# Kernel tuning notes

Hardware: AMD Instinct MI355X
Metric: run time of the kernel (lower is better)

The kernel has to match this reference:

```python
import jax, jax.numpy as jnp
import numpy as np

N_CELLS, N_GENES, N_EDGES, D = 10000, 2000, 4000000, 64


def setup_inputs() -> dict:
    key = jax.random.key(0)
    ks = jax.random.split(key, 10)
    return {
        "c_feat": jax.random.normal(ks[0], (N_CELLS, D), dtype=jnp.float32),
        "g_feat": jax.random.normal(ks[1], (N_GENES, D), dtype=jnp.float32),
        "cs_factor": jax.random.uniform(ks[2], (N_CELLS, 1), dtype=jnp.float32),
        "gs_factor": jax.random.uniform(ks[3], (N_GENES, 1), dtype=jnp.float32),
        "src": jax.random.randint(ks[4], (N_EDGES,), 0, N_CELLS),
        "dst": jax.random.randint(ks[5], (N_EDGES,), 0, N_GENES),
        "Wm": jax.random.normal(ks[6], (D, 1), dtype=jnp.float32) / np.sqrt(D),
        "bm": jnp.zeros((1,), dtype=jnp.float32),
        "Wd": jax.random.normal(ks[7], (D, 1), dtype=jnp.float32) / np.sqrt(D),
        "bd": jnp.zeros((1,), dtype=jnp.float32),
        "Wp": jax.random.normal(ks[8], (D, 1), dtype=jnp.float32) / np.sqrt(D),
        "bp": jnp.zeros((1,), dtype=jnp.float32),
    }


def reference(c_feat, g_feat, cs_factor, gs_factor, src, dst, Wm, bm, Wd, bd, Wp, bp):
    # Per-edge gather + elementwise product: u_mul_v('h','h','h_d')  -> [E, D]
    h_d = c_feat[src] * g_feat[dst]
    # Per-edge broadcast of node factors: gs from dst gene, cs from src cell -> [E, 1]
    gs = gs_factor[dst]
    cs = cs_factor[src]
    # Tiny Linear(D,1) heads
    mu_ = jax.nn.sigmoid(h_d @ Wm + bm)          # dec_mean
    disp_ = h_d @ Wd + bd                        # dec_disp
    pi = jax.nn.sigmoid(h_d @ Wp + bp)           # dec_pi
    # ZINB activations with clamping
    disp = jnp.clip(jax.nn.softplus(gs * disp_), 1e-4, 1e4)   # DispAct
    mu = cs * jnp.clip(jnp.exp(gs * mu_) - 1.0, 1e-5, 1e6)    # MeanAct scaled by cs
    return (mu, disp, pi)
```

## Files before the change

kernel.cpp:

```cpp
#include <hip/hip_runtime.h>
#include <hip/hip_bf16.h>
#include <hip/hip_fp16.h>


typedef unsigned int u32;
typedef unsigned short u16;
typedef long long i64;
typedef _Float16 v2h __attribute__((ext_vector_type(2)));

__device__ __forceinline__ float us2f(u16 u) { union { u32 i; float f; } v; v.i = ((u32)u) << 16; return v.f; }
__device__ __forceinline__ float lo2f(u32 u) { union { u32 i; float f; } v; v.i = u << 16; return v.f; }
__device__ __forceinline__ float hi2f(u32 u) { union { u32 i; float f; } v; v.i = u & 0xffff0000u; return v.f; }

union H2 { u32 u; __half2 h; v2h v; };

#if defined(__has_builtin)
#if __has_builtin(__builtin_amdgcn_fdot2)
#define HAS_FDOT2 1
#endif
#endif

__device__ __forceinline__ float qadd(float x) {
    int a = __builtin_amdgcn_mov_dpp(__float_as_int(x), 0xB1, 0xF, 0xF, true);
    float s = x + __int_as_float(a);
    int b = __builtin_amdgcn_mov_dpp(__float_as_int(s), 0x4E, 0xF, 0xF, true);
    return s + __int_as_float(b);
}

#define FLAGS_OFF 200
#define WHALF_B   1024
#define CS32_B    2048
#define GS32_B    42048
#define CHALF_B   50176
#define GHALF_B   1330176
#define WS_NEED   1586176

__global__ __launch_bounds__(256) void zinb_prep_all(
    const void* __restrict__ c, const void* __restrict__ g,
    const void* __restrict__ cs, const void* __restrict__ gsp,
    const void* __restrict__ src, const void* __restrict__ dst,
    const void* __restrict__ Wm, const void* __restrict__ bm,
    const void* __restrict__ Wd, const void* __restrict__ bd,
    const void* __restrict__ Wp, const void* __restrict__ bp,
    char* __restrict__ wsb, int nc, int ng, int ncs, int ngs, int E)
{
    __shared__ int sf[12];
    int t = threadIdx.x;
    if (t < 12) sf[t] = 0;
    __syncthreads();
    {
        int bad;
        const u32* pc = (const u32*)c;
        bad = 0; for (int i = t; i < 1024; i += 256) { int ex = (pc[i] >> 7) & 0xFF; if (ex >= 135) bad = 1; }
        if (bad) atomicOr(&sf[0], 1);
        const u32* pg = (const u32*)g;
        bad = 0; for (int i = t; i < 1024; i += 256) { int ex = (pg[i] >> 7) & 0xFF; if (ex >= 135) bad = 1; }
        if (bad) atomicOr(&sf[1], 1);
        const u32* ps = (const u32*)cs;
        bad = 0; for (int i = t; i < 1024; i += 256) { int ex = (ps[i] >> 7) & 0xFF; if (ex >= 135) bad = 1; }
        if (bad) atomicOr(&sf[2], 1);
        const u32* pq = (const u32*)gsp;
        bad = 0; for (int i = t; i < 1000; i += 256) { int ex = (pq[i] >> 7) & 0xFF; if (ex >= 135) bad = 1; }
        if (bad) atomicOr(&sf[3], 1);
        const u32* p4 = (const u32*)src;
        int on = 0, en = 0;
        for (int i = t; i < 1024; i += 256) { if (p4[2 * i + 1] != 0) on = 1; if (p4[2 * i] != 0) en = 1; }
        if (on) atomicOr(&sf[4], 1);
        if (en) atomicOr(&sf[5], 1);
        const u32* p5 = (const u32*)dst;
        on = 0; en = 0;
        for (int i = t; i < 1024; i += 256) { if (p5[2 * i + 1] != 0) on = 1; if (p5[2 * i] != 0) en = 1; }
        if (on) atomicOr(&sf[6], 1);
        if (en) atomicOr(&sf[7], 1);
        if (t < 3) {
            const u32* pw = (t == 0) ? (const u32*)Wm : (t == 1) ? (const u32*)Wd : (const u32*)Wp;
            bad = 0; for (int i = 0; i < 32; ++i) { int ex = (pw[i] >> 7) & 0xFF; if (ex >= 135) bad = 1; }
            if (bad) atomicOr(&sf[8 + t], 1);
        }
    }
    __syncthreads();
    int fc = sf[0], fg = sf[1], fcs = sf[2], fgs = sf[3];

    int i = blockIdx.x * 256 + t;
    __half* ch  = (__half*)(wsb + CHALF_B);
    __half* gh  = (__half*)(wsb + GHALF_B);
    float* cs32 = (float*)(wsb + CS32_B);
    float* gs32 = (float*)(wsb + GS32_B);
    if (i < nc) ch[i] = __float2half(fc ? ((const float*)c)[i] : us2f(((const u16*)c)[i]));
    if (i < ng) gh[i] = __float2half(fg ? ((const float*)g)[i] : us2f(((const u16*)g)[i]));
    if (i < ncs) cs32[i] = fcs ? ((const float*)cs)[i] : us2f(((const u16*)cs)[i]);
    if (i < ngs) gs32[i] = fgs ? ((const float*)gsp)[i] : us2f(((const u16*)gsp)[i]);

    if (blockIdx.x == 0) {
        float* W32 = (float*)wsb;
        int w0 = sf[8], w1 = sf[9], w2 = sf[10];
        if (t < 64) {
            W32[t]       = w0 ? ((const float*)Wm)[t] : us2f(((const u16*)Wm)[t]);
            W32[64 + t]  = w1 ? ((const float*)Wd)[t] : us2f(((const u16*)Wd)[t]);
            W32[128 + t] = w2 ? ((const float*)Wp)[t] : us2f(((const u16*)Wp)[t]);
        } else if (t == 64) {
            W32[192] = w0 ? ((const float*)bm)[0] : us2f(((const u16*)bm)[0]);
            W32[193] = w1 ? ((const float*)bd)[0] : us2f(((const u16*)bd)[0]);
            W32[194] = w2 ? ((const float*)bp)[0] : us2f(((const u16*)bp)[0]);
        }
        __syncthreads();
        __half* wh = (__half*)(wsb + WHALF_B);
        if (t < 192) wh[t] = __float2half(W32[t]);
        if (t == 192) {
            int* flg = (int*)wsb + FLAGS_OFF;
            flg[0] = fc; flg[1] = fg; flg[2] = fcs; flg[3] = fgs;
            flg[4] = (!sf[4] && sf[5]) ? 1 : 0;
            flg[5] = (!sf[6] && sf[7]) ? 1 : 0;
        }
    }
}

__device__ __forceinline__ void slice_dot(const uint4& c0, const uint4& c1,
                                          const uint4& g0, const uint4& g1,
                                          const u32* wm, const u32* wd, const u32* wp,
                                          float& am, float& ad, float& ap) {
    u32 cw[8] = {c0.x, c0.y, c0.z, c0.w, c1.x, c1.y, c1.z, c1.w};
    u32 gw[8] = {g0.x, g0.y, g0.z, g0.w, g1.x, g1.y, g1.z, g1.w};
    am = 0.f; ad = 0.f; ap = 0.f;
    #pragma unroll
    for (int j = 0; j < 8; ++j) {
        H2 a, b, pr, w;
        a.u = cw[j]; b.u = gw[j];
        pr.h = __hmul2(a.h, b.h);
#ifdef HAS_FDOT2
        w.u = wm[j]; am = __builtin_amdgcn_fdot2(pr.v, w.v, am, false);
        w.u = wd[j]; ad = __builtin_amdgcn_fdot2(pr.v, w.v, ad, false);
        w.u = wp[j]; ap = __builtin_amdgcn_fdot2(pr.v, w.v, ap, false);
#else
        float2 pf = __half22float2(pr.h);
        H2 t0, t1, t2; t0.u = wm[j]; t1.u = wd[j]; t2.u = wp[j];
        float2 wmf = __half22float2(t0.h);
        float2 wdf = __half22float2(t1.h);
        float2 wpf = __half22float2(t2.h);
        am = fmaf(pf.x, wmf.x, fmaf(pf.y, wmf.y, am));
        ad = fmaf(pf.x, wdf.x, fmaf(pf.y, wdf.y, ad));
        ap = fmaf(pf.x, wpf.x, fmaf(pf.y, wpf.y, ap));
#endif
    }
}

__device__ __forceinline__ void zinb_epilogue(float Sm, float Sd, float Sp,
                                              float cs, float gs,
                                              float bmv, float bdv, float bpv,
                                              float* out, int E, int e) {
    float mu_ = __builtin_amdgcn_rcpf(1.f + __expf(-(Sm + bmv)));
    float pi  = __builtin_amdgcn_rcpf(1.f + __expf(-(Sp + bpv)));
    float xd  = gs * (Sd + bdv);
    float sp  = fmaxf(xd, 0.f) + __logf(1.f + __expf(-fabsf(xd)));
    float disp = fminf(fmaxf(sp, 1e-4f), 1e4f);
    float em  = __expf(gs * mu_) - 1.f;
    float mu  = cs * fminf(fmaxf(em, 1e-5f), 1e6f);
    out[e]         = mu;
    out[E + e]     = disp;
    out[2 * E + e] = pi;
}

__global__ __launch_bounds__(256) void zinb_fast3(
    const __half* __restrict__ cT, const __half* __restrict__ gT,
    const float* __restrict__ cs32, const float* __restrict__ gs32,
    const void* __restrict__ src, const void* __restrict__ dst,
    const char* __restrict__ wsb, float* __restrict__ out, int E)
{
    const float* W32 = (const float*)wsb;
    const int* flags = (const int*)wsb + FLAGS_OFF;
    int fs64 = flags[4], fd64 = flags[5];

    int tid = threadIdx.x;
    int q = tid >> 2, l = tid & 3;
    int base = blockIdx.x * 256;

    int sI[4], dI[4];
    #pragma unroll
    for (int it = 0; it < 4; ++it) {
        int e = base + it * 64 + q;
        sI[it] = fs64 ? (int)((const i64*)src)[e] : ((const int*)src)[e];
        dI[it] = fd64 ? (int)((const i64*)dst)[e] : ((const int*)dst)[e];
    }
    int s_own = sI[0], d_own = dI[0];
    #pragma unroll
    for (int it = 1; it < 4; ++it) {
        if (l == it) { s_own = sI[it]; d_own = dI[it]; }
    }
    float cs = cs32[s_own];
    float gs = gs32[d_own];

    const uint4* Wh = (const uint4*)(wsb + WHALF_B);
    uint4 m0 = Wh[l],      m1 = Wh[4 + l];
    uint4 d0 = Wh[8 + l],  d1 = Wh[12 + l];
    uint4 p0 = Wh[16 + l], p1 = Wh[20 + l];
    u32 wm[8] = {m0.x, m0.y, m0.z, m0.w, m1.x, m1.y, m1.z, m1.w};
    u32 wd[8] = {d0.x, d0.y, d0.z, d0.w, d1.x, d1.y, d1.z, d1.w};
    u32 wp[8] = {p0.x, p0.y, p0.z, p0.w, p1.x, p1.y, p1.z, p1.w};
    float bmv = W32[192], bdv = W32[193], bpv = W32[194];

    const uint4* cr = (const uint4*)(cT + (size_t)sI[0] * 64);
    const uint4* gr = (const uint4*)(gT + (size_t)dI[0] * 64);
    uint4 c0 = cr[l], c1 = cr[4 + l];
    uint4 g0 = gr[l], g1 = gr[4 + l];

    float Sm = 0.f, Sd = 0.f, Sp = 0.f;
    #pragma unroll
    for (int it = 0; it < 4; ++it) {
        uint4 nc0, nc1, ng0, ng1;
        if (it < 3) {
            const uint4* crn = (const uint4*)(cT + (size_t)sI[it + 1] * 64);
            const uint4* grn = (const uint4*)(gT + (size_t)dI[it + 1] * 64);
            nc0 = crn[l]; nc1 = crn[4 + l];
            ng0 = grn[l]; ng1 = grn[4 + l];
        }
        float am, ad, ap;
        slice_dot(c0, c1, g0, g1, wm, wd, wp, am, ad, ap);
        am = qadd(am); ad = qadd(ad); ap = qadd(ap);
        if (l == it) { Sm = am; Sd = ad; Sp = ap; }
        if (it < 3) { c0 = nc0; c1 = nc1; g0 = ng0; g1 = ng1; }
    }

    int e_own = base + l * 64 + q;
    zinb_epilogue(Sm, Sd, Sp, cs, gs, bmv, bdv, bpv, out, E, e_own);
}

__global__ __launch_bounds__(256) void zinb_fast2t(
    const __half* __restrict__ cT, const __half* __restrict__ gT,
    const float* __restrict__ cs32, const float* __restrict__ gs32,
    const void* __restrict__ src, const void* __restrict__ dst,
    const char* __restrict__ wsb, float* __restrict__ out, int E, int base0)
{
    const float* W32 = (const float*)wsb;
    const int* flags = (const int*)wsb + FLAGS_OFF;
    int fs64 = flags[4], fd64 = flags[5];

    int tid = threadIdx.x;
    int q = tid >> 2, l = tid & 3;
    int base = base0 + blockIdx.x * 256;

    const uint4* Wh = (const uint4*)(wsb + WHALF_B);
    uint4 m0 = Wh[l],      m1 = Wh[4 + l];
    uint4 d0 = Wh[8 + l],  d1 = Wh[12 + l];
    uint4 p0 = Wh[16 + l], p1 = Wh[20 + l];
    u32 wm[8] = {m0.x, m0.y, m0.z, m0.w, m1.x, m1.y, m1.z, m1.w};
    u32 wd[8] = {d0.x, d0.y, d0.z, d0.w, d1.x, d1.y, d1.z, d1.w};
    u32 wp[8] = {p0.x, p0.y, p0.z, p0.w, p1.x, p1.y, p1.z, p1.w};
    float bmv = W32[192], bdv = W32[193], bpv = W32[194];

    float Sm = 0.f, Sd = 0.f, Sp = 0.f;
    int ss = 0, sd2 = 0, se = -1;

    #pragma unroll
    for (int it = 0; it < 4; ++it) {
        int e = base + it * 64 + q;
        bool ok = (e < E);
        int s = 0, d = 0;
        float am = 0.f, ad = 0.f, ap = 0.f;
        if (ok) {
            s = fs64 ? (int)((const i64*)src)[e] : ((const int*)src)[e];
            d = fd64 ? (int)((const i64*)dst)[e] : ((const int*)dst)[e];
            const uint4* cr = (const uint4*)(cT + (size_t)s * 64);
            const uint4* gr = (const uint4*)(gT + (size_t)d * 64);
            uint4 c0 = cr[l], c1 = cr[4 + l];
            uint4 g0 = gr[l], g1 = gr[4 + l];
            slice_dot(c0, c1, g0, g1, wm, wd, wp, am, ad, ap);
        }
        am = qadd(am); ad = qadd(ad); ap = qadd(ap);
        if (l == it && ok) { Sm = am; Sd = ad; Sp = ap; ss = s; sd2 = d; se = e; }
    }

    if (se >= 0)
        zinb_epilogue(Sm, Sd, Sp, cs32[ss], gs32[sd2], bmv, bdv, bpv, out, E, se);
}

__global__ void zinb_detect(const void* c, int nc, const void* g, int ng,
                            const void* cs, int ncs, const void* gsp, int ngs,
                            const void* src, int ns, const void* dst, int nd,
                            int* flags) {
    __shared__ int s_a, s_b;
    int b = blockIdx.x, t = threadIdx.x;
    if (t == 0) { s_a = 0; s_b = 0; }
    __syncthreads();
    if (b < 4) {
        const u32* p; int n;
        if (b == 0)      { p = (const u32*)c;   n = nc;  }
        else if (b == 1) { p = (const u32*)g;   n = ng;  }
        else if (b == 2) { p = (const u32*)cs;  n = ncs; }
        else             { p = (const u32*)gsp; n = ngs; }
        int words = n / 2; if (words > 16384) words = 16384;
        int bad = 0;
        for (int i = t; i < words; i += 256) { int ex = (p[i] >> 7) & 0xFF; if (ex >= 135) bad = 1; }
        if (bad) atomicOr(&s_a, 1);
        __syncthreads();
        if (t == 0) flags[b] = s_a;
    } else {
        const u32* p = (b == 4) ? (const u32*)src : (const u32*)dst;
        int n = (b == 4) ? ns : nd;
        int pairs = (n < 4096) ? n / 2 : 2048;
        int oddnz = 0, evennz = 0;
        for (int i = t; i < pairs; i += 256) {
            if (p[2 * i + 1] != 0) oddnz = 1;
            if (p[2 * i] != 0)     evennz = 1;
        }
        if (oddnz)  atomicOr(&s_a, 1);
        if (evennz) atomicOr(&s_b, 1);
        __syncthreads();
        if (t == 0) flags[b] = (!s_a && s_b) ? 1 : 0;
    }
}

__global__ void zinb_prep_w(const void* Wm, const void* bm, const void* Wd,
                            const void* bd, const void* Wp, const void* bp,
                            float* W) {
    __shared__ int wf[3];
    int t = threadIdx.x;
    if (t < 3) {
        const u32* p = (t == 0) ? (const u32*)Wm : (t == 1) ? (const u32*)Wd : (const u32*)Wp;
        int bad = 0;
        for (int i = 0; i < 32; ++i) { int ex = (p[i] >> 7) & 0xFF; if (ex >= 135) bad = 1; }
        wf[t] = bad;
    }
    __syncthreads();
    if (t < 64) {
        W[t]       = wf[0] ? ((const float*)Wm)[t] : us2f(((const u16*)Wm)[t]);
        W[64 + t]  = wf[1] ? ((const float*)Wd)[t] : us2f(((const u16*)Wd)[t]);
        W[128 + t] = wf[2] ? ((const float*)Wp)[t] : us2f(((const u16*)Wp)[t]);
    } else if (t == 64) {
        W[192] = wf[0] ? ((const float*)bm)[0] : us2f(((const u16*)bm)[0]);
        W[193] = wf[1] ? ((const float*)bd)[0] : us2f(((const u16*)bd)[0]);
        W[194] = wf[2] ? ((const float*)bp)[0] : us2f(((const u16*)bp)[0]);
    }
}

__global__ __launch_bounds__(256) void zinb_main(
    const void* __restrict__ c_feat, const void* __restrict__ g_feat,
    const void* __restrict__ cs_f, const void* __restrict__ gs_f,
    const void* __restrict__ src, const void* __restrict__ dst,
    const float* __restrict__ W, float* __restrict__ out, int E)
{
    int e = blockIdx.x * 256 + threadIdx.x;
    if (e >= E) return;
    const int* flags = (const int*)W + FLAGS_OFF;
    int fc = flags[0], fg = flags[1], fcs = flags[2], fgs = flags[3];
    int fs64 = flags[4], fd64 = flags[5];
    int s = fs64 ? (int)((const i64*)src)[e] : ((const int*)src)[e];
    int d = fd64 ? (int)((const i64*)dst)[e] : ((const int*)dst)[e];
    const char* crow = (const char*)c_feat + (size_t)s * (fc ? 256 : 128);
    const char* grow = (const char*)g_feat + (size_t)d * (fg ? 256 : 128);
    float accm = 0.f, accd = 0.f, accp = 0.f;
    for (int ch = 0; ch < 4; ++ch) {
        float cb[16], gb[16];
        if (fc) {
            const float4* qq = (const float4*)crow;
            #pragma unroll
            for (int j4 = 0; j4 < 4; ++j4) {
                float4 v = qq[ch * 4 + j4];
                cb[j4 * 4] = v.x; cb[j4 * 4 + 1] = v.y; cb[j4 * 4 + 2] = v.z; cb[j4 * 4 + 3] = v.w;
            }
        } else {
            const uint4* qq = (const uint4*)crow;
            #pragma unroll
            for (int j2 = 0; j2 < 2; ++j2) {
                uint4 v = qq[ch * 2 + j2];
                u32 w[4] = {v.x, v.y, v.z, v.w};
                #pragma unroll
                for (int j = 0; j < 4; ++j) {
                    cb[j2 * 8 + j * 2] = lo2f(w[j]); cb[j2 * 8 + j * 2 + 1] = hi2f(w[j]);
                }
            }
        }
        if (fg) {
            const float4* qq = (const float4*)grow;
            #pragma unroll
            for (int j4 = 0; j4 < 4; ++j4) {
                float4 v = qq[ch * 4 + j4];
                gb[j4 * 4] = v.x; gb[j4 * 4 + 1] = v.y; gb[j4 * 4 + 2] = v.z; gb[j4 * 4 + 3] = v.w;
            }
        } else {
            const uint4* qq = (const uint4*)grow;
            #pragma unroll
            for (int j2 = 0; j2 < 2; ++j2) {
                uint4 v = qq[ch * 2 + j2];
                u32 w[4] = {v.x, v.y, v.z, v.w};
                #pragma unroll
                for (int j = 0; j < 4; ++j) {
                    gb[j2 * 8 + j * 2] = lo2f(w[j]); gb[j2 * 8 + j * 2 + 1] = hi2f(w[j]);
                }
            }
        }
        #pragma unroll
        for (int j = 0; j < 16; ++j) {
            int k = ch * 16 + j;
            float h = cb[j] * gb[j];
            accm = fmaf(h, W[k], accm);
            accd = fmaf(h, W[64 + k], accd);
            accp = fmaf(h, W[128 + k], accp);
        }
    }
    float cs = fcs ? ((const float*)cs_f)[s] : us2f(((const u16*)cs_f)[s]);
    float gs = fgs ? ((const float*)gs_f)[d] : us2f(((const u16*)gs_f)[d]);
    float bmv = W[192], bdv = W[193], bpv = W[194];
    float mu_ = 1.f / (1.f + expf(-(accm + bmv)));
    float pi  = 1.f / (1.f + expf(-(accp + bpv)));
    float xd  = gs * (accd + bdv);
    float sp  = fmaxf(xd, 0.f) + log1pf(expf(-fabsf(xd)));
    float disp = fminf(fmaxf(sp, 1e-4f), 1e4f);
    float em  = expf(gs * mu_) - 1.f;
    float mu  = cs * fminf(fmaxf(em, 1e-5f), 1e6f);
    out[e] = mu; out[E + e] = disp; out[2 * E + e] = pi;
}

extern "C" void kernel_launch(void* const* d_in, const int* in_sizes, int n_in,
                              void* d_out, int out_size, void* d_ws, size_t ws_size,
                              hipStream_t stream) {
    const void* c_feat = d_in[0];
    const void* g_feat = d_in[1];
    const void* cs_f   = d_in[2];
    const void* gs_f   = d_in[3];
    const void* src    = d_in[4];
    const void* dst    = d_in[5];
    const void* Wm     = d_in[6];
    const void* bm     = d_in[7];
    const void* Wd     = d_in[8];
    const void* bd     = d_in[9];
    const void* Wp     = d_in[10];
    const void* bp     = d_in[11];

    int E = in_sizes[4];
    int nc = in_sizes[0], ng = in_sizes[1], ncs = in_sizes[2], ngs = in_sizes[3];
    char* wsb = (char*)d_ws;

    if (ws_size >= (size_t)WS_NEED) {
        int nmax = nc > ng ? nc : ng;
        int prep_blocks = (nmax + 255) / 256;
        zinb_prep_all<<<prep_blocks, 256, 0, stream>>>(
            c_feat, g_feat, cs_f, gs_f, src, dst,
            Wm, bm, Wd, bd, Wp, bp, wsb, nc, ng, ncs, ngs, E);

        const __half* cT = (const __half*)(wsb + CHALF_B);
        const __half* gT = (const __half*)(wsb + GHALF_B);
        const float* cs32 = (const float*)(wsb + CS32_B);
        const float* gs32 = (const float*)(wsb + GS32_B);

        int full_blocks = E / 256;
        if (full_blocks > 0)
            zinb_fast3<<<full_blocks, 256, 0, stream>>>(cT, gT, cs32, gs32, src, dst,
                                                        wsb, (float*)d_out, E);
        int tail = E - full_blocks * 256;
        if (tail > 0)
            zinb_fast2t<<<1, 256, 0, stream>>>(cT, gT, cs32, gs32, src, dst,
                                               wsb, (float*)d_out, E, full_blocks * 256);
    } else {
        float* W = (float*)d_ws;
        int* flags = (int*)W + FLAGS_OFF;
        zinb_detect<<<6, 256, 0, stream>>>(c_feat, nc, g_feat, ng, cs_f, ncs,
                                           gs_f, ngs, src, E, dst, in_sizes[5], flags);
        zinb_prep_w<<<1, 256, 0, stream>>>(Wm, bm, Wd, bd, Wp, bp, W);
        int blocks = (E + 255) / 256;
        zinb_main<<<blocks, 256, 0, stream>>>(c_feat, g_feat, cs_f, gs_f, src, dst,
                                              W, (float*)d_out, E);
    }
}
```

Measured before the change: 195.3 us.

## Split prep into detect/vectorized convert, fp16 scale factors, 4 tiles per block

Replaces the combined prep kernel with a single-block detect kernel and a separate vectorized conversion kernel that converts four elements per thread. Cell and gene scale factors are now stored as fp16 instead of fp32. The main kernel processes four 256-edge tiles per block to amortize weight loading and reduce block count. This adds a kernel launch and reduces precision of the scale factors, which may affect accuracy.

```diff
diff --git a/kernel.cpp b/kernel.cpp
--- a/kernel.cpp
+++ b/kernel.cpp
@@ -29,20 +29,20 @@
 
 #define FLAGS_OFF 200
 #define WHALF_B   1024
-#define CS32_B    2048
-#define GS32_B    42048
-#define CHALF_B   50176
-#define GHALF_B   1330176
-#define WS_NEED   1586176
-
-__global__ __launch_bounds__(256) void zinb_prep_all(
+#define CSH_B     2048
+#define GSH_B     22528
+#define CHALF_B   28672
+#define GHALF_B   1308672
+#define WS_NEED   1564672
+
+__global__ __launch_bounds__(256) void zinb_detect1(
     const void* __restrict__ c, const void* __restrict__ g,
     const void* __restrict__ cs, const void* __restrict__ gsp,
     const void* __restrict__ src, const void* __restrict__ dst,
     const void* __restrict__ Wm, const void* __restrict__ bm,
     const void* __restrict__ Wd, const void* __restrict__ bd,
     const void* __restrict__ Wp, const void* __restrict__ bp,
-    char* __restrict__ wsb, int nc, int ng, int ncs, int ngs, int E)
+    char* __restrict__ wsb, int ngs)
 {
     __shared__ int sf[12];
     int t = threadIdx.x;
@@ -60,7 +60,8 @@
         bad = 0; for (int i = t; i < 1024; i += 256) { int ex = (ps[i] >> 7) & 0xFF; if (ex >= 135) bad = 1; }
         if (bad) atomicOr(&sf[2], 1);
         const u32* pq = (const u32*)gsp;
-        bad = 0; for (int i = t; i < 1000; i += 256) { int ex = (pq[i] >> 7) & 0xFF; if (ex >= 135) bad = 1; }
+        int wq = ngs / 2; if (wq > 1000) wq = 1000;
+        bad = 0; for (int i = t; i < wq; i += 256) { int ex = (pq[i] >> 7) & 0xFF; if (ex >= 135) bad = 1; }
         if (bad) atomicOr(&sf[3], 1);
         const u32* p4 = (const u32*)src;
         int on = 0, en = 0;
@@ -79,40 +80,64 @@
         }
     }
     __syncthreads();
-    int fc = sf[0], fg = sf[1], fcs = sf[2], fgs = sf[3];
-
-    int i = blockIdx.x * 256 + t;
-    __half* ch  = (__half*)(wsb + CHALF_B);
-    __half* gh  = (__half*)(wsb + GHALF_B);
-    float* cs32 = (float*)(wsb + CS32_B);
-    float* gs32 = (float*)(wsb + GS32_B);
-    if (i < nc) ch[i] = __float2half(fc ? ((const float*)c)[i] : us2f(((const u16*)c)[i]));
-    if (i < ng) gh[i] = __float2half(fg ? ((const float*)g)[i] : us2f(((const u16*)g)[i]));
-    if (i < ncs) cs32[i] = fcs ? ((const float*)cs)[i] : us2f(((const u16*)cs)[i]);
-    if (i < ngs) gs32[i] = fgs ? ((const float*)gsp)[i] : us2f(((const u16*)gsp)[i]);
-
-    if (blockIdx.x == 0) {
-        float* W32 = (float*)wsb;
-        int w0 = sf[8], w1 = sf[9], w2 = sf[10];
-        if (t < 64) {
-            W32[t]       = w0 ? ((const float*)Wm)[t] : us2f(((const u16*)Wm)[t]);
-            W32[64 + t]  = w1 ? ((const float*)Wd)[t] : us2f(((const u16*)Wd)[t]);
-            W32[128 + t] = w2 ? ((const float*)Wp)[t] : us2f(((const u16*)Wp)[t]);
-        } else if (t == 64) {
-            W32[192] = w0 ? ((const float*)bm)[0] : us2f(((const u16*)bm)[0]);
-            W32[193] = w1 ? ((const float*)bd)[0] : us2f(((const u16*)bd)[0]);
-            W32[194] = w2 ? ((const float*)bp)[0] : us2f(((const u16*)bp)[0]);
-        }
-        __syncthreads();
-        __half* wh = (__half*)(wsb + WHALF_B);
-        if (t < 192) wh[t] = __float2half(W32[t]);
-        if (t == 192) {
-            int* flg = (int*)wsb + FLAGS_OFF;
-            flg[0] = fc; flg[1] = fg; flg[2] = fcs; flg[3] = fgs;
-            flg[4] = (!sf[4] && sf[5]) ? 1 : 0;
-            flg[5] = (!sf[6] && sf[7]) ? 1 : 0;
-        }
-    }
+    float* W32 = (float*)wsb;
+    int w0 = sf[8], w1 = sf[9], w2 = sf[10];
+    if (t < 64) {
+        W32[t]       = w0 ? ((const float*)Wm)[t] : us2f(((const u16*)Wm)[t]);
+        W32[64 + t]  = w1 ? ((const float*)Wd)[t] : us2f(((const u16*)Wd)[t]);
+        W32[128 + t] = w2 ? ((const float*)Wp)[t] : us2f(((const u16*)Wp)[t]);
+    } else if (t == 64) {
+        W32[192] = w0 ? ((const float*)bm)[0] : us2f(((const u16*)bm)[0]);
+        W32[193] = w1 ? ((const float*)bd)[0] : us2f(((const u16*)bd)[0]);
+        W32[194] = w2 ? ((const float*)bp)[0] : us2f(((const u16*)bp)[0]);
+    }
+    __syncthreads();
+    __half* wh = (__half*)(wsb + WHALF_B);
+    if (t < 192) wh[t] = __float2half(W32[t]);
+    if (t == 192) {
+        int* flg = (int*)wsb + FLAGS_OFF;
+        flg[0] = sf[0]; flg[1] = sf[1]; flg[2] = sf[2]; flg[3] = sf[3];
+        flg[4] = (!sf[4] && sf[5]) ? 1 : 0;
+        flg[5] = (!sf[6] && sf[7]) ? 1 : 0;
+    }
+}
+
+__device__ __forceinline__ void cvt4(const void* p, int fp32, int i4, __half* dst) {
+    H2 a, b;
+    if (fp32) {
+        float4 v = ((const float4*)p)[i4 >> 2];
+        a.h = __floats2half2_rn(v.x, v.y);
+        b.h = __floats2half2_rn(v.z, v.w);
+    } else {
+        uint2 u = ((const uint2*)p)[i4 >> 2];
+        a.h = __floats2half2_rn(lo2f(u.x), hi2f(u.x));
+        b.h = __floats2half2_rn(lo2f(u.y), hi2f(u.y));
+    }
+    uint2 o; o.x = a.u; o.y = b.u;
+    ((uint2*)dst)[i4 >> 2] = o;
+}
+
+__global__ __launch_bounds__(256) void zinb_convert4(
+    const void* __restrict__ c, const void* __restrict__ g,
+    const void* __restrict__ cs, const void* __restrict__ gsp,
+    char* __restrict__ wsb, int nc, int ng, int ncs, int ngs)
+{
+    const int* flg = (const int*)wsb + FLAGS_OFF;
+    int fc = flg[0], fg = flg[1], fcs = flg[2], fgs = flg[3];
+    int t = blockIdx.x * 256 + threadIdx.x;
+    int i4 = t * 4;
+    __half* ch = (__half*)(wsb + CHALF_B);
+    __half* gh = (__half*)(wsb + GHALF_B);
+    if (i4 + 3 < nc) cvt4(c, fc, i4, ch);
+    else for (int k = 0; k < 4; ++k) if (i4 + k < nc)
+        ch[i4 + k] = __float2half(fc ? ((const float*)c)[i4 + k] : us2f(((const u16*)c)[i4 + k]));
+    if (i4 + 3 < ng) cvt4(g, fg, i4, gh);
+    else for (int k = 0; k < 4; ++k) if (i4 + k < ng)
+        gh[i4 + k] = __float2half(fg ? ((const float*)g)[i4 + k] : us2f(((const u16*)g)[i4 + k]));
+    __half* csh = (__half*)(wsb + CSH_B);
+    __half* gsh = (__half*)(wsb + GSH_B);
+    if (t < ncs) csh[t] = __float2half(fcs ? ((const float*)cs)[t] : us2f(((const u16*)cs)[t]));
+    if (t < ngs) gsh[t] = __float2half(fgs ? ((const float*)gsp)[t] : us2f(((const u16*)gsp)[t]));
 }
 
 __device__ __forceinline__ void slice_dot(const uint4& c0, const uint4& c1,
@@ -160,9 +185,9 @@
     out[2 * E + e] = pi;
 }
 
-__global__ __launch_bounds__(256) void zinb_fast3(
+__global__ __launch_bounds__(256) void zinb_fast4(
     const __half* __restrict__ cT, const __half* __restrict__ gT,
-    const float* __restrict__ cs32, const float* __restrict__ gs32,
+    const __half* __restrict__ csh, const __half* __restrict__ gsh,
     const void* __restrict__ src, const void* __restrict__ dst,
     const char* __restrict__ wsb, float* __restrict__ out, int E)
 {
@@ -172,22 +197,6 @@
 
     int tid = threadIdx.x;
     int q = tid >> 2, l = tid & 3;
-    int base = blockIdx.x * 256;
-
-    int sI[4], dI[4];
-    #pragma unroll
-    for (int it = 0; it < 4; ++it) {
-        int e = base + it * 64 + q;
-        sI[it] = fs64 ? (int)((const i64*)src)[e] : ((const int*)src)[e];
-        dI[it] = fd64 ? (int)((const i64*)dst)[e] : ((const int*)dst)[e];
-    }
-    int s_own = sI[0], d_own = dI[0];
-    #pragma unroll
-    for (int it = 1; it < 4; ++it) {
-        if (l == it) { s_own = sI[it]; d_own = dI[it]; }
-    }
-    float cs = cs32[s_own];
-    float gs = gs32[d_own];
 
     const uint4* Wh = (const uint4*)(wsb + WHALF_B);
     uint4 m0 = Wh[l],      m1 = Wh[4 + l];
@@ -198,35 +207,56 @@
     u32 wp[8] = {p0.x, p0.y, p0.z, p0.w, p1.x, p1.y, p1.z, p1.w};
     float bmv = W32[192], bdv = W32[193], bpv = W32[194];
 
-    const uint4* cr = (const uint4*)(cT + (size_t)sI[0] * 64);
-    const uint4* gr = (const uint4*)(gT + (size_t)dI[0] * 64);
-    uint4 c0 = cr[l], c1 = cr[4 + l];
-    uint4 g0 = gr[l], g1 = gr[4 + l];
-
-    float Sm = 0.f, Sd = 0.f, Sp = 0.f;
+    int blockBase = blockIdx.x * 1024;
+
     #pragma unroll
-    for (int it = 0; it < 4; ++it) {
-        uint4 nc0, nc1, ng0, ng1;
-        if (it < 3) {
-            const uint4* crn = (const uint4*)(cT + (size_t)sI[it + 1] * 64);
-            const uint4* grn = (const uint4*)(gT + (size_t)dI[it + 1] * 64);
-            nc0 = crn[l]; nc1 = crn[4 + l];
-            ng0 = grn[l]; ng1 = grn[4 + l];
-        }
-        float am, ad, ap;
-        slice_dot(c0, c1, g0, g1, wm, wd, wp, am, ad, ap);
-        am = qadd(am); ad = qadd(ad); ap = qadd(ap);
-        if (l == it) { Sm = am; Sd = ad; Sp = ap; }
-        if (it < 3) { c0 = nc0; c1 = nc1; g0 = ng0; g1 = ng1; }
-    }
-
-    int e_own = base + l * 64 + q;
-    zinb_epilogue(Sm, Sd, Sp, cs, gs, bmv, bdv, bpv, out, E, e_own);
+    for (int tile = 0; tile < 4; ++tile) {
+        int base = blockBase + tile * 256;
+
+        int sI[4], dI[4];
+        #pragma unroll
+        for (int it = 0; it < 4; ++it) {
+            int e = base + it * 64 + q;
+            sI[it] = fs64 ? (int)((const i64*)src)[e] : ((const int*)src)[e];
+            dI[it] = fd64 ? (int)((const i64*)dst)[e] : ((const int*)dst)[e];
+        }
+        int s_own = sI[0], d_own = dI[0];
+        #pragma unroll
+        for (int it = 1; it < 4; ++it)
+            if (l == it) { s_own = sI[it]; d_own = dI[it]; }
+        float cs = __half2float(csh[s_own]);
+        float gs = __half2float(gsh[d_own]);
+
+        const uint4* cr = (const uint4*)(cT + (size_t)sI[0] * 64);
+        const uint4* gr = (const uint4*)(gT + (size_t)dI[0] * 64);
+        uint4 c0 = cr[l], c1 = cr[4 + l];
+        uint4 g0 = gr[l], g1 = gr[4 + l];
+
+        float Sm = 0.f, Sd = 0.f, Sp = 0.f;
+        #pragma unroll
+        for (int it = 0; it < 4; ++it) {
+            uint4 nc0, nc1, ng0, ng1;
+            if (it < 3) {
+                const uint4* crn = (const uint4*)(cT + (size_t)sI[it + 1] * 64);
+                const uint4* grn = (const uint4*)(gT + (size_t)dI[it + 1] * 64);
+                nc0 = crn[l]; nc1 = crn[4 + l];
+                ng0 = grn[l]; ng1 = grn[4 + l];
+            }
+            float am, ad, ap;
+            slice_dot(c0, c1, g0, g1, wm, wd, wp, am, ad, ap);
+            am = qadd(am); ad = qadd(ad); ap = qadd(ap);
+            if (l == it) { Sm = am; Sd = ad; Sp = ap; }
+            if (it < 3) { c0 = nc0; c1 = nc1; g0 = ng0; g1 = ng1; }
+        }
+
+        int e_own = base + l * 64 + q;
+        zinb_epilogue(Sm, Sd, Sp, cs, gs, bmv, bdv, bpv, out, E, e_own);
+    }
 }
 
 __global__ __launch_bounds__(256) void zinb_fast2t(
     const __half* __restrict__ cT, const __half* __restrict__ gT,
-    const float* __restrict__ cs32, const float* __restrict__ gs32,
+    const __half* __restrict__ csh, const __half* __restrict__ gsh,
     const void* __restrict__ src, const void* __restrict__ dst,
     const char* __restrict__ wsb, float* __restrict__ out, int E, int base0)
 {
@@ -270,7 +300,8 @@
     }
 
     if (se >= 0)
-        zinb_epilogue(Sm, Sd, Sp, cs32[ss], gs32[sd2], bmv, bdv, bpv, out, E, se);
+        zinb_epilogue(Sm, Sd, Sp, __half2float(csh[ss]), __half2float(gsh[sd2]),
+                      bmv, bdv, bpv, out, E, se);
 }
 
 __global__ void zinb_detect(const void* c, int nc, const void* g, int ng,
@@ -431,25 +462,28 @@
     char* wsb = (char*)d_ws;
 
     if (ws_size >= (size_t)WS_NEED) {
-        int nmax = nc > ng ? nc : ng;
-        int prep_blocks = (nmax + 255) / 256;
-        zinb_prep_all<<<prep_blocks, 256, 0, stream>>>(
-            c_feat, g_feat, cs_f, gs_f, src, dst,
-            Wm, bm, Wd, bd, Wp, bp, wsb, nc, ng, ncs, ngs, E);
-
-        const __half* cT = (const __half*)(wsb + CHALF_B);
-        const __half* gT = (const __half*)(wsb + GHALF_B);
-        const float* cs32 = (const float*)(wsb + CS32_B);
-        const float* gs32 = (const float*)(wsb + GS32_B);
-
-        int full_blocks = E / 256;
-        if (full_blocks > 0)
-            zinb_fast3<<<full_blocks, 256, 0, stream>>>(cT, gT, cs32, gs32, src, dst,
-                                                        wsb, (float*)d_out, E);
-        int tail = E - full_blocks * 256;
-        if (tail > 0)
-            zinb_fast2t<<<1, 256, 0, stream>>>(cT, gT, cs32, gs32, src, dst,
-                                               wsb, (float*)d_out, E, full_blocks * 256);
+        zinb_detect1<<<1, 256, 0, stream>>>(c_feat, g_feat, cs_f, gs_f, src, dst,
+                                            Wm, bm, Wd, bd, Wp, bp, wsb, ngs);
+        int nmax4 = ((nc > ng ? nc : ng) + 3) / 4;
+        int nmax = nmax4 > ncs ? nmax4 : ncs;
+        nmax = nmax > ngs ? nmax : ngs;
+        int cvt_blocks = (nmax + 255) / 256;
+        zinb_convert4<<<cvt_blocks, 256, 0, stream>>>(c_feat, g_feat, cs_f, gs_f,
+                                                      wsb, nc, ng, ncs, ngs);
+
+        const __half* cT  = (const __half*)(wsb + CHALF_B);
+        const __half* gT  = (const __half*)(wsb + GHALF_B);
+        const __half* csh = (const __half*)(wsb + CSH_B);
+        const __half* gsh = (const __half*)(wsb + GSH_B);
+
+        int full1024 = E / 1024;
+        if (full1024 > 0)
+            zinb_fast4<<<full1024, 256, 0, stream>>>(cT, gT, csh, gsh, src, dst,
+                                                     wsb, (float*)d_out, E);
+        int rem = E - full1024 * 1024;
+        if (rem > 0)
+            zinb_fast2t<<<(rem + 255) / 256, 256, 0, stream>>>(
+                cT, gT, csh, gsh, src, dst, wsb, (float*)d_out, E, full1024 * 1024);
     } else {
         float* W = (float*)d_ws;
         int* flags = (int*)W + FLAGS_OFF;
```

Result: slower. 203.7 us (+4.3%).
